# Kernel optimization log

Measured on AMD Instinct MI355X. Metric: run time of the kernel, lower is better.

The kernel has to match this reference:

```python
import jax, jax.numpy as jnp
import numpy as np

D_MODEL, D_STATE, D_CONV, EXPAND = 1024, 16, 4, 2
D_INNER = EXPAND * D_MODEL            # 2048
DT_RANK = -(-D_MODEL // 16)           # ceil(d_model/16) = 64


def setup_inputs() -> dict:
    key = jax.random.key(0)
    ks = jax.random.split(key, 9)
    B, L = 2, 2048
    x = jax.random.normal(ks[0], (B, L, D_MODEL), dtype=jnp.float32)
    s = 0.02
    W_in = jax.random.normal(ks[1], (2 * D_INNER, D_MODEL), dtype=jnp.float32) * s
    conv_w = jax.random.normal(ks[2], (D_INNER, 1, D_CONV), dtype=jnp.float32) * 0.1
    conv_b = jax.random.normal(ks[3], (D_INNER,), dtype=jnp.float32) * 0.01
    W_xproj = jax.random.normal(ks[4], (DT_RANK + 2 * D_STATE, D_INNER), dtype=jnp.float32) * s
    W_dt = jax.random.normal(ks[5], (D_INNER, DT_RANK), dtype=jnp.float32) * (DT_RANK ** -0.5)
    b_dt = jnp.log(jnp.exp(jax.random.uniform(ks[6], (D_INNER,), minval=1e-3, maxval=0.1)) - 1.0)  # inv-softplus init
    A_log = jnp.log(jnp.broadcast_to(jnp.arange(1, D_STATE + 1, dtype=jnp.float32), (D_INNER, D_STATE)))
    Dskip = jnp.ones((D_INNER,), dtype=jnp.float32)
    W_out = jax.random.normal(ks[7], (D_MODEL, D_INNER), dtype=jnp.float32) * s
    return {"x": x, "W_in": W_in, "conv_w": conv_w, "conv_b": conv_b,
            "W_xproj": W_xproj, "W_dt": W_dt, "b_dt": b_dt,
            "A_log": A_log, "Dskip": Dskip, "W_out": W_out}


def _mamba_fwd(x, W_in, conv_w, conv_b, W_xproj, W_dt, b_dt, A_log, Dskip, W_out):
    Bsz, L, _ = x.shape
    # in_proj -> split into x branch and gate z
    xz = jnp.einsum('bld,ed->ble', x, W_in)               # (B,L,2*d_inner)
    xb, z = jnp.split(xz, 2, axis=-1)
    # causal depthwise conv1d over time
    xc = jnp.transpose(xb, (0, 2, 1))                      # (B,d_inner,L)
    xc = jax.lax.conv_general_dilated(
        xc, conv_w, window_strides=(1,), padding=[(D_CONV - 1, 0)],
        dimension_numbers=('NCH', 'OIH', 'NCH'), feature_group_count=D_INNER)
    u = jax.nn.silu(jnp.transpose(xc, (0, 2, 1)) + conv_b)  # (B,L,d_inner)
    # input-dependent SSM params
    x_dbl = jnp.einsum('bld,ed->ble', u, W_xproj)          # (B,L,dt_rank+2n)
    dt_low, Bmat, Cmat = jnp.split(x_dbl, [DT_RANK, DT_RANK + D_STATE], axis=-1)
    delta = jax.nn.softplus(jnp.einsum('blr,dr->bld', dt_low, W_dt) + b_dt)  # (B,L,d_inner)
    A = -jnp.exp(A_log)                                    # (d_inner,d_state)

    def step(h, inp):
        dt_t, u_t, B_t, C_t = inp                          # (B,d),(B,d),(B,n),(B,n)
        dA = jnp.exp(dt_t[:, :, None] * A)                 # (B,d,n)
        h = dA * h + (dt_t * u_t)[:, :, None] * B_t[:, None, :]
        y_t = jnp.einsum('bdn,bn->bd', h, C_t)
        return h, y_t

    h0 = jnp.zeros((Bsz, D_INNER, D_STATE), dtype=x.dtype)
    xs = (jnp.transpose(delta, (1, 0, 2)), jnp.transpose(u, (1, 0, 2)),
          jnp.transpose(Bmat, (1, 0, 2)), jnp.transpose(Cmat, (1, 0, 2)))
    _, ys = jax.lax.scan(step, h0, xs)                     # (L,B,d_inner)
    y = jnp.transpose(ys, (1, 0, 2)) + u * Dskip           # skip connection
    y = y * jax.nn.silu(z)                                 # gating
    return jnp.einsum('bld,ed->ble', y, W_out)             # (B,L,d_model)


def reference(x, W_in, conv_w, conv_b, W_xproj, W_dt, b_dt, A_log, Dskip, W_out):
    return _mamba_fwd(x, W_in, conv_w, conv_b, W_xproj, W_dt, b_dt, A_log, Dskip, W_out)
```

## Files before the change

kernel.cpp:

```cpp
#include <hip/hip_runtime.h>
#include <math.h>

#define MB_B      2
#define MB_L      2048
#define MB_DMODEL 1024
#define MB_DINNER 2048
#define MB_DSTATE 16
#define MB_DTRANK 64
#define MB_ROWS   (MB_B * MB_L)
#define MB_E2     (2 * MB_DINNER)
#define SC_NC     32
#define SC_CHUNK  (MB_L / SC_NC)
#define SC_CL     32
#define SC_CB     64
#define CV_R      4

typedef _Float16 f16;
typedef __attribute__((ext_vector_type(2))) _Float16 half2v;
typedef __attribute__((ext_vector_type(4))) _Float16 half4;
typedef __attribute__((ext_vector_type(8))) _Float16 half8;
typedef __attribute__((ext_vector_type(4))) float floatx4;

__device__ __forceinline__ float softplus_f(float x) {
    return (x > 20.f) ? x : log1pf(expf(x));
}
__device__ __forceinline__ float silu_f(float x) {
    return x / (1.f + expf(-x));
}

#if __has_builtin(__builtin_amdgcn_exp2f)
__device__ __forceinline__ float exp2_fast(float x) {
    return __builtin_amdgcn_exp2f(x);
}
#else
__device__ __forceinline__ float exp2_fast(float x) {
    return __expf(0.69314718056f * x);
}
#endif

typedef const __attribute__((address_space(1))) unsigned char gbyte;
typedef __attribute__((address_space(3))) unsigned char lbyte;
__device__ __forceinline__ void gl_lds16(const void* g, void* l) {
    __builtin_amdgcn_global_load_lds((gbyte*)g, (lbyte*)l, 16, 0, 0);
}

template <int CTRL>
__device__ __forceinline__ float dpp_add(float x) {
    int xi = __builtin_bit_cast(int, x);
    int yi = __builtin_amdgcn_update_dpp(0, xi, CTRL, 0xF, 0xF, true);
    return x + __builtin_bit_cast(float, yi);
}

__global__ __launch_bounds__(256) void convert_all_kernel(
    const float* __restrict__ x, const float* __restrict__ W_in,
    const float* __restrict__ W_xproj, const float* __restrict__ W_dt,
    const float* __restrict__ W_out, f16* __restrict__ dst)
{
    const int i = (blockIdx.x * 256 + threadIdx.x) * 8;
    const float* src;
    int local, nsrc;
    if (i < 4194304)      { src = x;       local = i;           nsrc = 4194304; }
    else if (i < 8388608) { src = W_in;    local = i - 4194304; nsrc = 4194304; }
    else if (i < 8650752) { src = W_xproj; local = i - 8388608; nsrc = 196608; }
    else if (i < 8781824) { src = W_dt;    local = i - 8650752; nsrc = 131072; }
    else                  { src = W_out;   local = i - 8781824; nsrc = 2097152; }
    half8 o;
    if (local < nsrc) {
        const float4 a = *reinterpret_cast<const float4*>(src + local);
        const float4 b = *reinterpret_cast<const float4*>(src + local + 4);
        o[0] = (f16)a.x; o[1] = (f16)a.y; o[2] = (f16)a.z; o[3] = (f16)a.w;
        o[4] = (f16)b.x; o[5] = (f16)b.y; o[6] = (f16)b.z; o[7] = (f16)b.w;
    } else {
#pragma unroll
        for (int j = 0; j < 8; j++) o[j] = (f16)0.f;
    }
    *reinterpret_cast<half8*>(dst + i) = o;
}

template <typename OutT, int EPI, int BM, int GN>
__global__ __launch_bounds__(256) void gemm_mfma(
    const f16* __restrict__ A, int lda,
    const f16* __restrict__ B, int ldb,
    OutT* __restrict__ C, int ldc, int K,
    const float* __restrict__ bias)
{
    constexpr int BN = 128;
    constexpr int GM = 4 / GN;
    constexpr int WM = BM / GM;
    constexpr int WN = BN / GN;
    constexpr int MT = WM / 16, NT = WN / 16;
    constexpr int CPW = (BM + BN) / 32;

    __shared__ f16 As[BM * 64];
    __shared__ f16 Bs[BN * 64];

    const int tid  = threadIdx.x;
    const int lane = tid & 63;
    const int wave = tid >> 6;
    const int wr   = wave / GN, wc = wave % GN;
    const int bm   = blockIdx.y * BM, bn = blockIdx.x * BN;

    floatx4 zero4 = {0.f, 0.f, 0.f, 0.f};
    floatx4 acc[MT][NT];
#pragma unroll
    for (int i = 0; i < MT; i++)
#pragma unroll
        for (int j = 0; j < NT; j++) acc[i][j] = zero4;

    const int srow = lane >> 3;
    const int scol = ((lane & 7) ^ (srow & 7)) * 8;
    const f16* gp[CPW];
    f16* lp[CPW];
#pragma unroll
    for (int i = 0; i < CPW; i++) {
        const int rbase = (wave * CPW + i) * 8;
        if (rbase < BM) {
            gp[i] = A + (size_t)(bm + rbase + srow) * lda + scol;
            lp[i] = As + rbase * 64;
        } else {
            gp[i] = B + (size_t)(bn + (rbase - BM) + srow) * ldb + scol;
            lp[i] = Bs + (rbase - BM) * 64;
        }
    }

    const int mr = lane & 15;
    const int ko = lane >> 4;

    for (int k0 = 0; k0 < K; k0 += 64) {
#pragma unroll
        for (int i = 0; i < CPW; i++) gl_lds16(gp[i] + k0, lp[i]);
        __syncthreads();

        half8 af[MT][2], bf[NT][2];
#pragma unroll
        for (int kk = 0; kk < 2; kk++) {
            const int koff = ((ko + kk * 4) ^ (mr & 7)) * 8;
#pragma unroll
            for (int mt = 0; mt < MT; mt++)
                af[mt][kk] = *reinterpret_cast<const half8*>(
                    As + (wr * WM + mt * 16 + mr) * 64 + koff);
#pragma unroll
            for (int nt = 0; nt < NT; nt++)
                bf[nt][kk] = *reinterpret_cast<const half8*>(
                    Bs + (wc * WN + nt * 16 + mr) * 64 + koff);
        }
#pragma unroll
        for (int kk = 0; kk < 2; kk++)
#pragma unroll
            for (int mt = 0; mt < MT; mt++)
#pragma unroll
                for (int nt = 0; nt < NT; nt++)
                    acc[mt][nt] = __builtin_amdgcn_mfma_f32_16x16x32_f16(
                        af[mt][kk], bf[nt][kk], acc[mt][nt], 0, 0, 0);
        __syncthreads();
    }

    const int rbase = (lane >> 4) * 4;
#pragma unroll
    for (int mt = 0; mt < MT; mt++) {
        const int row0 = bm + wr * WM + mt * 16 + rbase;
#pragma unroll
        for (int nt = 0; nt < NT; nt++) {
            const int col = bn + wc * WN + nt * 16 + mr;
#pragma unroll
            for (int r = 0; r < 4; r++) {
                float v = acc[mt][nt][r];
                if constexpr (EPI == 1) v = softplus_f(v + bias[col]);
                C[(size_t)(row0 + r) * ldc + col] = (OutT)v;
            }
        }
    }
}

__global__ __launch_bounds__(256) void gemm3_splitk(
    const f16* __restrict__ A, const f16* __restrict__ B,
    float* __restrict__ Cp)
{
    __shared__ f16 As[128 * 32];
    __shared__ f16 Bs[128 * 32];

    const int tid  = threadIdx.x;
    const int lane = tid & 63;
    const int wave = tid >> 6;
    const int wr   = wave >> 1, wc = wave & 1;
    const int bm   = blockIdx.y * 128;
    const int kbeg = blockIdx.x * 256;

    floatx4 zero4 = {0.f, 0.f, 0.f, 0.f};
    floatx4 acc[4][4];
#pragma unroll
    for (int i = 0; i < 4; i++)
#pragma unroll
        for (int j = 0; j < 4; j++) acc[i][j] = zero4;

    const int srow = lane >> 2;
    const int scol = ((lane & 3) ^ ((srow >> 1) & 3)) * 8;
    const f16* gA0 = A + (size_t)(bm + wave * 32 + srow) * MB_DINNER + scol;
    const f16* gA1 = A + (size_t)(bm + wave * 32 + 16 + srow) * MB_DINNER + scol;
    const f16* gB0 = B + (size_t)(wave * 32 + srow) * MB_DINNER + scol;
    const f16* gB1 = B + (size_t)(wave * 32 + 16 + srow) * MB_DINNER + scol;
    f16* lA0 = As + wave * 1024;
    f16* lA1 = As + wave * 1024 + 512;
    f16* lB0 = Bs + wave * 1024;
    f16* lB1 = Bs + wave * 1024 + 512;

    const int mr = lane & 15;
    const int kq = ((lane >> 4) ^ ((mr >> 1) & 3)) * 8;

    for (int k0 = kbeg; k0 < kbeg + 256; k0 += 32) {
        gl_lds16(gA0 + k0, lA0);
        gl_lds16(gA1 + k0, lA1);
        gl_lds16(gB0 + k0, lB0);
        gl_lds16(gB1 + k0, lB1);
        __syncthreads();

        half8 af[4], bf[4];
#pragma unroll
        for (int mt = 0; mt < 4; mt++)
            af[mt] = *reinterpret_cast<const half8*>(
                As + (wr * 64 + mt * 16 + mr) * 32 + kq);
#pragma unroll
        for (int nt = 0; nt < 4; nt++)
            bf[nt] = *reinterpret_cast<const half8*>(
                Bs + (wc * 64 + nt * 16 + mr) * 32 + kq);
#pragma unroll
        for (int mt = 0; mt < 4; mt++)
#pragma unroll
            for (int nt = 0; nt < 4; nt++)
                acc[mt][nt] = __builtin_amdgcn_mfma_f32_16x16x32_f16(
                    af[mt], bf[nt], acc[mt][nt], 0, 0, 0);
        __syncthreads();
    }

    float* Co = Cp + (size_t)blockIdx.x * MB_ROWS * 128;
    const int rbase = (lane >> 4) * 4;
#pragma unroll
    for (int mt = 0; mt < 4; mt++) {
        const int row0 = bm + wr * 64 + mt * 16 + rbase;
#pragma unroll
        for (int nt = 0; nt < 4; nt++) {
            const int col = wc * 64 + nt * 16 + mr;
#pragma unroll
            for (int r = 0; r < 4; r++)
                Co[(size_t)(row0 + r) * 128 + col] = acc[mt][nt][r];
        }
    }
}

__global__ __launch_bounds__(256) void reduce_xdbl_kernel(
    const float* __restrict__ Cp, float* __restrict__ xdbl,
    f16* __restrict__ xdbl_h)
{
    const int t = blockIdx.x * 256 + threadIdx.x;
    const int row = t >> 5, c4 = (t & 31) * 4;
    float4 s = {0.f, 0.f, 0.f, 0.f};
#pragma unroll
    for (int j = 0; j < 8; j++) {
        const float4 v = *reinterpret_cast<const float4*>(
            Cp + (size_t)j * MB_ROWS * 128 + (size_t)row * 128 + c4);
        s.x += v.x; s.y += v.y; s.z += v.z; s.w += v.w;
    }
    if (c4 < 96)
        *reinterpret_cast<float4*>(xdbl + (size_t)row * 96 + c4) = s;
    half4 h = {(f16)s.x, (f16)s.y, (f16)s.z, (f16)s.w};
    *reinterpret_cast<half4*>(xdbl_h + (size_t)row * 128 + c4) = h;
}

__global__ __launch_bounds__(256) void conv_silu_kernel(
    const f16* __restrict__ xz, const float* __restrict__ cw,
    const float* __restrict__ cb, f16* __restrict__ u)
{
    const int tid  = threadIdx.x;
    const int dv   = tid * 8;
    const int rbeg = blockIdx.x * CV_R;
    const int l0   = rbeg & (MB_L - 1);

    float wt[8][4];
#pragma unroll
    for (int j = 0; j < 8; j++) {
        const float4 wv = *reinterpret_cast<const float4*>(cw + (dv + j) * 4);
        wt[j][0] = wv.x; wt[j][1] = wv.y; wt[j][2] = wv.z; wt[j][3] = wv.w;
    }
    float bias[8];
    {
        const float4 b0 = *reinterpret_cast<const float4*>(cb + dv);
        const float4 b1 = *reinterpret_cast<const float4*>(cb + dv + 4);
        bias[0] = b0.x; bias[1] = b0.y; bias[2] = b0.z; bias[3] = b0.w;
        bias[4] = b1.x; bias[5] = b1.y; bias[6] = b1.z; bias[7] = b1.w;
    }

    half8 xr[CV_R + 3];
#pragma unroll
    for (int i = 0; i < 3; i++) {
        if (l0 >= 3 - i) {
            xr[i] = *reinterpret_cast<const half8*>(
                xz + (size_t)(rbeg - 3 + i) * MB_E2 + dv);
        } else {
#pragma unroll
            for (int j = 0; j < 8; j++) xr[i][j] = (f16)0.f;
        }
    }
#pragma unroll
    for (int r = 0; r < CV_R; r++)
        xr[3 + r] = *reinterpret_cast<const half8*>(
            xz + (size_t)(rbeg + r) * MB_E2 + dv);

#pragma unroll
    for (int r = 0; r < CV_R; r++) {
        float acc[8];
#pragma unroll
        for (int j = 0; j < 8; j++) acc[j] = bias[j];
#pragma unroll
        for (int k = 0; k < 4; k++) {
            const half8 xv = xr[r + k];
#pragma unroll
            for (int j = 0; j < 8; j++)
                acc[j] = fmaf((float)xv[j], wt[j][k], acc[j]);
        }
        half8 o;
#pragma unroll
        for (int j = 0; j < 8; j++) o[j] = (f16)silu_f(acc[j]);
        *reinterpret_cast<half8*>(u + (size_t)(rbeg + r) * MB_DINNER + dv) = o;
    }
}

__global__ __launch_bounds__(256) void scan_pass1(
    const f16*  __restrict__ delta,
    const f16*  __restrict__ u,
    const float* __restrict__ xdbl,
    const float* __restrict__ A_log,
    float* __restrict__ Hc,
    float* __restrict__ Pc)
{
    __shared__ half2v sDU[SC_CB][SC_CL + 2];
    __shared__ float  sB[SC_CL][20];

    const int tid   = threadIdx.x;
    const int lane  = tid & 63;
    const int wave  = tid >> 6;
    const int cg    = (lane >> 2) & 15;
    const int q     = lane & 3;
    const int ch    = wave * 16 + cg;
    const int cb    = blockIdx.x & 63;
    const int chunk = blockIdx.x >> 6;
    const int gchan = cb * SC_CB + ch;
    const int b     = gchan >> 11;
    const int dbase = (cb & 31) * SC_CB;
    const int d     = dbase + ch;
    const int lbeg  = chunk * SC_CHUNK;

    const size_t base2048 = (size_t)b * MB_L * MB_DINNER;
    const size_t base96   = (size_t)b * MB_L * 96;

    const float4 alog = *reinterpret_cast<const float4*>(
        A_log + d * MB_DSTATE + q * 4);
    float Av2[4] = {-expf(alog.x) * 1.44269504f, -expf(alog.y) * 1.44269504f,
                    -expf(alog.z) * 1.44269504f, -expf(alog.w) * 1.44269504f};
    float h[4] = {0.f, 0.f, 0.f, 0.f};
    float sdt = 0.f;

    const int lloc  = tid >> 3;
    const int c8    = (tid & 7) * 8;
    const int cpair = (tid & 7) * 2;

    half8 pD, pU; float2 pB;
    auto stage_load = [&](int l0) {
        const size_t row = (size_t)(l0 + lloc);
        pD = *reinterpret_cast<const half8*>(
            delta + base2048 + row * MB_DINNER + dbase + c8);
        pU = *reinterpret_cast<const half8*>(
            u + base2048 + row * MB_DINNER + dbase + c8);
        pB = *reinterpret_cast<const float2*>(
            xdbl + base96 + row * 96 + MB_DTRANK + cpair);
    };
    auto stage_write = [&]() {
#pragma unroll
        for (int j = 0; j < 8; j++) {
            half2v t; t[0] = pD[j]; t[1] = pD[j] * pU[j];
            sDU[c8 + j][lloc] = t;
        }
        *reinterpret_cast<float2*>(&sB[lloc][cpair]) = pB;
    };

    stage_load(lbeg);
    stage_write();
    __syncthreads();

    for (int l0 = lbeg; l0 < lbeg + SC_CHUNK; l0 += SC_CL) {
        const bool has_next = (l0 + SC_CL) < lbeg + SC_CHUNK;
        if (has_next) stage_load(l0 + SC_CL);

#pragma unroll
        for (int ll = 0; ll < SC_CL; ll++) {
            const half2v duh = sDU[ch][ll];
            const float dx = (float)duh[0], dy = (float)duh[1];
            const float4 Bv = *reinterpret_cast<const float4*>(&sB[ll][q * 4]);
            h[0] = fmaf(exp2_fast(dx * Av2[0]), h[0], dy * Bv.x);
            h[1] = fmaf(exp2_fast(dx * Av2[1]), h[1], dy * Bv.y);
            h[2] = fmaf(exp2_fast(dx * Av2[2]), h[2], dy * Bv.z);
            h[3] = fmaf(exp2_fast(dx * Av2[3]), h[3], dy * Bv.w);
            sdt += dx;
        }
        __syncthreads();
        if (has_next) stage_write();
        __syncthreads();
    }

    const size_t cidx = ((size_t)chunk * MB_ROWS + gchan) * MB_DSTATE + q * 4;
    float4 H4 = {h[0], h[1], h[2], h[3]};
    float4 P4 = {exp2_fast(Av2[0] * sdt), exp2_fast(Av2[1] * sdt),
                 exp2_fast(Av2[2] * sdt), exp2_fast(Av2[3] * sdt)};
    *reinterpret_cast<float4*>(Hc + cidx) = H4;
    *reinterpret_cast<float4*>(Pc + cidx) = P4;
}

__global__ __launch_bounds__(256) void scan_pass2(
    const f16*  __restrict__ delta,
    const f16*  __restrict__ u,
    const float* __restrict__ xdbl,
    const float* __restrict__ A_log,
    const float* __restrict__ Dskip,
    const f16*  __restrict__ xz,
    const float* __restrict__ Hc,
    const float* __restrict__ Pc,
    f16* __restrict__ yg)
{
    __shared__ half2v sDU[SC_CB][SC_CL + 2];
    __shared__ half2v sGS[SC_CB][SC_CL + 2];
    __shared__ float  sB[SC_CL][20];
    __shared__ float  sC[SC_CL][20];

    const int tid   = threadIdx.x;
    const int lane  = tid & 63;
    const int wave  = tid >> 6;
    const int cg    = (lane >> 2) & 15;
    const int q     = lane & 3;
    const int ch    = wave * 16 + cg;
    const int cb    = blockIdx.x & 63;
    const int chunk = blockIdx.x >> 6;
    const int gchan = cb * SC_CB + ch;
    const int b     = gchan >> 11;
    const int dbase = (cb & 31) * SC_CB;
    const int d     = dbase + ch;
    const int lbeg  = chunk * SC_CHUNK;

    const size_t base2048 = (size_t)b * MB_L * MB_DINNER;
    const size_t base4096 = (size_t)b * MB_L * MB_E2;
    const size_t base96   = (size_t)b * MB_L * 96;

    const float4 alog = *reinterpret_cast<const float4*>(
        A_log + d * MB_DSTATE + q * 4);
    float Av2[4] = {-expf(alog.x) * 1.44269504f, -expf(alog.y) * 1.44269504f,
                    -expf(alog.z) * 1.44269504f, -expf(alog.w) * 1.44269504f};

    const int lloc  = tid >> 3;
    const int c8    = (tid & 7) * 8;
    const int cpair = (tid & 7) * 2;

    float Dsk8[8];
    {
        const float4 d0 = *reinterpret_cast<const float4*>(Dskip + dbase + c8);
        const float4 d1 = *reinterpret_cast<const float4*>(Dskip + dbase + c8 + 4);
        Dsk8[0] = d0.x; Dsk8[1] = d0.y; Dsk8[2] = d0.z; Dsk8[3] = d0.w;
        Dsk8[4] = d1.x; Dsk8[5] = d1.y; Dsk8[6] = d1.z; Dsk8[7] = d1.w;
    }

    half8 pD, pU, pZ; float2 pB, pC;
    auto stage_load = [&](int l0) {
        const size_t row = (size_t)(l0 + lloc);
        pD = *reinterpret_cast<const half8*>(
            delta + base2048 + row * MB_DINNER + dbase + c8);
        pU = *reinterpret_cast<const half8*>(
            u + base2048 + row * MB_DINNER + dbase + c8);
        pZ = *reinterpret_cast<const half8*>(
            xz + base4096 + row * MB_E2 + MB_DINNER + dbase + c8);
        pB = *reinterpret_cast<const float2*>(
            xdbl + base96 + row * 96 + MB_DTRANK + cpair);
        pC = *reinterpret_cast<const float2*>(
            xdbl + base96 + row * 96 + MB_DTRANK + MB_DSTATE + cpair);
    };
    auto stage_write = [&]() {
#pragma unroll
        for (int j = 0; j < 8; j++) {
            half2v t; t[0] = pD[j]; t[1] = pD[j] * pU[j];
            sDU[c8 + j][lloc] = t;
            const float uu = (float)pU[j];
            const float g = silu_f((float)pZ[j]);
            half2v gs; gs[0] = (f16)g; gs[1] = (f16)(uu * Dsk8[j] * g);
            sGS[c8 + j][lloc] = gs;
        }
        *reinterpret_cast<float2*>(&sB[lloc][cpair]) = pB;
        *reinterpret_cast<float2*>(&sC[lloc][cpair]) = pC;
    };

    stage_load(lbeg);

    float h[4] = {0.f, 0.f, 0.f, 0.f};
    for (int j = 0; j < chunk; j++) {
        const size_t cidx = ((size_t)j * MB_ROWS + gchan) * MB_DSTATE + q * 4;
        const float4 P4 = *reinterpret_cast<const float4*>(Pc + cidx);
        const float4 H4 = *reinterpret_cast<const float4*>(Hc + cidx);
        h[0] = fmaf(P4.x, h[0], H4.x);
        h[1] = fmaf(P4.y, h[1], H4.y);
        h[2] = fmaf(P4.z, h[2], H4.z);
        h[3] = fmaf(P4.w, h[3], H4.w);
    }

    stage_write();
    __syncthreads();

    for (int l0 = lbeg; l0 < lbeg + SC_CHUNK; l0 += SC_CL) {
        const bool has_next = (l0 + SC_CL) < lbeg + SC_CHUNK;
        if (has_next) stage_load(l0 + SC_CL);

        float y[SC_CL / 4] = {0.f, 0.f, 0.f, 0.f, 0.f, 0.f, 0.f, 0.f};
#pragma unroll
        for (int ll = 0; ll < SC_CL; ll++) {
            const half2v duh = sDU[ch][ll];
            const float dx = (float)duh[0], dy = (float)duh[1];
            const float4 Bv = *reinterpret_cast<const float4*>(&sB[ll][q * 4]);
            const float4 Cv = *reinterpret_cast<const float4*>(&sC[ll][q * 4]);
            h[0] = fmaf(exp2_fast(dx * Av2[0]), h[0], dy * Bv.x);
            h[1] = fmaf(exp2_fast(dx * Av2[1]), h[1], dy * Bv.y);
            h[2] = fmaf(exp2_fast(dx * Av2[2]), h[2], dy * Bv.z);
            h[3] = fmaf(exp2_fast(dx * Av2[3]), h[3], dy * Bv.w);
            float p = h[0] * Cv.x;
            p = fmaf(h[1], Cv.y, p);
            p = fmaf(h[2], Cv.z, p);
            p = fmaf(h[3], Cv.w, p);
            p = dpp_add<0xB1>(p);
            p = dpp_add<0x4E>(p);
            y[ll >> 2] = (q == (ll & 3)) ? p : y[ll >> 2];
        }

#pragma unroll
        for (int k = 0; k < SC_CL / 4; k++) {
            const half2v gs = sGS[ch][4 * k + q];
            yg[base2048 + (size_t)(l0 + 4 * k + q) * MB_DINNER + dbase + ch] =
                (f16)fmaf(y[k], (float)gs[0], (float)gs[1]);
        }

        __syncthreads();
        if (has_next) stage_write();
        __syncthreads();
    }
}

extern "C" void kernel_launch(void* const* d_in, const int* in_sizes, int n_in,
                              void* d_out, int out_size, void* d_ws,
                              size_t ws_size, hipStream_t stream)
{
    const float* x      = (const float*)d_in[0];
    const float* W_in   = (const float*)d_in[1];
    const float* conv_w = (const float*)d_in[2];
    const float* conv_b = (const float*)d_in[3];
    const float* W_xproj= (const float*)d_in[4];
    const float* W_dt   = (const float*)d_in[5];
    const float* b_dt   = (const float*)d_in[6];
    const float* A_log  = (const float*)d_in[7];
    const float* Dskip  = (const float*)d_in[8];
    const float* W_out  = (const float*)d_in[9];
    float* out = (float*)d_out;

    char* p = (char*)d_ws;
    f16* xz_h    = (f16*)p;  p += (size_t)MB_ROWS * MB_E2 * 2;
    f16* u_h     = (f16*)p;  p += (size_t)MB_ROWS * MB_DINNER * 2;
    f16* delta_h = (f16*)p;  p += (size_t)MB_ROWS * MB_DINNER * 2;
    f16* yg_h    = (f16*)p;  p += (size_t)MB_ROWS * MB_DINNER * 2;
    float* xdbl  = (float*)p; p += (size_t)MB_ROWS * 96 * 4;
    f16* xdbl_h  = (f16*)p;  p += (size_t)MB_ROWS * 128 * 2;
    f16* x_h     = (f16*)p;  p += (size_t)MB_ROWS * MB_DMODEL * 2;
    f16* W_inh   = (f16*)p;  p += (size_t)MB_E2 * MB_DMODEL * 2;
    f16* W_xprojh= (f16*)p;  p += (size_t)128 * MB_DINNER * 2;
    f16* W_dth   = (f16*)p;  p += (size_t)MB_DINNER * MB_DTRANK * 2;
    f16* W_outh  = (f16*)p;  p += (size_t)MB_DMODEL * MB_DINNER * 2;
    float* Cp    = (float*)p;
    float* Hc    = Cp;
    float* Pc    = Cp + (size_t)SC_NC * MB_ROWS * MB_DSTATE;

    const dim3 blk(256);

    convert_all_kernel<<<5312, blk, 0, stream>>>(
        x, W_in, W_xproj, W_dt, W_out, x_h);

    gemm_mfma<f16, 0, 128, 2><<<dim3(32, 32), blk, 0, stream>>>(
        x_h, MB_DMODEL, W_inh, MB_DMODEL, xz_h, MB_E2, MB_DMODEL, nullptr);

    conv_silu_kernel<<<MB_ROWS / CV_R, blk, 0, stream>>>(
        xz_h, conv_w, conv_b, u_h);

    gemm3_splitk<<<dim3(8, 32), blk, 0, stream>>>(u_h, W_xprojh, Cp);
    reduce_xdbl_kernel<<<512, blk, 0, stream>>>(Cp, xdbl, xdbl_h);

    gemm_mfma<f16, 1, 128, 2><<<dim3(16, 32), blk, 0, stream>>>(
        xdbl_h, 128, W_dth, MB_DTRANK, delta_h, MB_DINNER, MB_DTRANK, b_dt);

    scan_pass1<<<(SC_NC - 1) * 64, blk, 0, stream>>>(
        delta_h, u_h, xdbl, A_log, Hc, Pc);

    scan_pass2<<<SC_NC * 64, blk, 0, stream>>>(
        delta_h, u_h, xdbl, A_log, Dskip, xz_h, Hc, Pc, yg_h);

    gemm_mfma<float, 0, 64, 4><<<dim3(8, 64), blk, 0, stream>>>(
        yg_h, MB_DINNER, W_outh, MB_DINNER, out, MB_DMODEL, MB_DINNER, nullptr);
}
```

Baseline: 308.7 us.

## Store split-K partials in fp16, split dt/BC outputs, remap in_proj block order

```diff
diff --git a/kernel.cpp b/kernel.cpp
--- a/kernel.cpp
+++ b/kernel.cpp
@@ -77,11 +77,11 @@
     *reinterpret_cast<half8*>(dst + i) = o;
 }
 
-template <typename OutT, int EPI, int BM, int GN>
+template <typename OutT, int EPI, int BM, int GN, int CMLOG>
 __global__ __launch_bounds__(256) void gemm_mfma(
     const f16* __restrict__ A, int lda,
     const f16* __restrict__ B, int ldb,
-    OutT* __restrict__ C, int ldc, int K,
+    OutT* __restrict__ C, int ldc, int kiters, long stepA, long stepB,
     const float* __restrict__ bias)
 {
     constexpr int BN = 128;
@@ -98,7 +98,16 @@
     const int lane = tid & 63;
     const int wave = tid >> 6;
     const int wr   = wave / GN, wc = wave % GN;
-    const int bm   = blockIdx.y * BM, bn = blockIdx.x * BN;
+
+    int bxi, byi;
+    if constexpr (CMLOG >= 0) {
+        const int n = blockIdx.x;
+        byi = ((n & 7) << CMLOG) | ((n >> 3) & ((1 << CMLOG) - 1));
+        bxi = n >> (3 + CMLOG);
+    } else {
+        bxi = blockIdx.x; byi = blockIdx.y;
+    }
+    const int bm = byi * BM, bn = bxi * BN;
 
     floatx4 zero4 = {0.f, 0.f, 0.f, 0.f};
     floatx4 acc[MT][NT];
@@ -111,24 +120,28 @@
     const int scol = ((lane & 7) ^ (srow & 7)) * 8;
     const f16* gp[CPW];
     f16* lp[CPW];
+    long stp[CPW];
 #pragma unroll
     for (int i = 0; i < CPW; i++) {
         const int rbase = (wave * CPW + i) * 8;
         if (rbase < BM) {
             gp[i] = A + (size_t)(bm + rbase + srow) * lda + scol;
             lp[i] = As + rbase * 64;
+            stp[i] = stepA;
         } else {
             gp[i] = B + (size_t)(bn + (rbase - BM) + srow) * ldb + scol;
             lp[i] = Bs + (rbase - BM) * 64;
+            stp[i] = stepB;
         }
     }
 
     const int mr = lane & 15;
     const int ko = lane >> 4;
 
-    for (int k0 = 0; k0 < K; k0 += 64) {
-#pragma unroll
-        for (int i = 0; i < CPW; i++) gl_lds16(gp[i] + k0, lp[i]);
+    for (int it = 0; it < kiters; it++) {
+#pragma unroll
+        for (int i = 0; i < CPW; i++)
+            gl_lds16(gp[i] + (size_t)((long)it * stp[i]), lp[i]);
         __syncthreads();
 
         half8 af[MT][2], bf[NT][2];
@@ -174,7 +187,7 @@
 
 __global__ __launch_bounds__(256) void gemm3_splitk(
     const f16* __restrict__ A, const f16* __restrict__ B,
-    float* __restrict__ Cp)
+    f16* __restrict__ Cp)
 {
     __shared__ f16 As[128 * 32];
     __shared__ f16 Bs[128 * 32];
@@ -232,7 +245,7 @@
         __syncthreads();
     }
 
-    float* Co = Cp + (size_t)blockIdx.x * MB_ROWS * 128;
+    f16* Co = Cp + (size_t)blockIdx.x * MB_ROWS * 128;
     const int rbase = (lane >> 4) * 4;
 #pragma unroll
     for (int mt = 0; mt < 4; mt++) {
@@ -242,28 +255,41 @@
             const int col = wc * 64 + nt * 16 + mr;
 #pragma unroll
             for (int r = 0; r < 4; r++)
-                Co[(size_t)(row0 + r) * 128 + col] = acc[mt][nt][r];
-        }
-    }
-}
-
-__global__ __launch_bounds__(256) void reduce_xdbl_kernel(
-    const float* __restrict__ Cp, float* __restrict__ xdbl,
-    f16* __restrict__ xdbl_h)
+                Co[(size_t)(row0 + r) * 128 + col] = (f16)acc[mt][nt][r];
+        }
+    }
+}
+
+__global__ __launch_bounds__(256) void reduce_bc_kernel(
+    const f16* __restrict__ Cp, f16* __restrict__ dt_h,
+    float* __restrict__ bc)
 {
     const int t = blockIdx.x * 256 + threadIdx.x;
-    const int row = t >> 5, c4 = (t & 31) * 4;
-    float4 s = {0.f, 0.f, 0.f, 0.f};
-#pragma unroll
-    for (int j = 0; j < 8; j++) {
-        const float4 v = *reinterpret_cast<const float4*>(
-            Cp + (size_t)j * MB_ROWS * 128 + (size_t)row * 128 + c4);
-        s.x += v.x; s.y += v.y; s.z += v.z; s.w += v.w;
-    }
-    if (c4 < 96)
-        *reinterpret_cast<float4*>(xdbl + (size_t)row * 96 + c4) = s;
-    half4 h = {(f16)s.x, (f16)s.y, (f16)s.z, (f16)s.w};
-    *reinterpret_cast<half4*>(xdbl_h + (size_t)row * 128 + c4) = h;
+    if (t < 65536) {
+        const int row = t >> 4, c4 = (t & 15) * 4;
+        float s[4] = {0.f, 0.f, 0.f, 0.f};
+#pragma unroll
+        for (int j = 0; j < 8; j++) {
+            const half4 v = *reinterpret_cast<const half4*>(
+                Cp + (size_t)j * MB_ROWS * 128 + (size_t)row * 128 + c4);
+            s[0] += (float)v[0]; s[1] += (float)v[1];
+            s[2] += (float)v[2]; s[3] += (float)v[3];
+        }
+        half4 h = {(f16)s[0], (f16)s[1], (f16)s[2], (f16)s[3]};
+        *reinterpret_cast<half4*>(dt_h + (size_t)row * 64 + c4) = h;
+    } else {
+        const int t2 = t - 65536;
+        const int row = t2 >> 3, c4 = (t2 & 7) * 4;
+        float4 s = {0.f, 0.f, 0.f, 0.f};
+#pragma unroll
+        for (int j = 0; j < 8; j++) {
+            const half4 v = *reinterpret_cast<const half4*>(
+                Cp + (size_t)j * MB_ROWS * 128 + (size_t)row * 128 + 64 + c4);
+            s.x += (float)v[0]; s.y += (float)v[1];
+            s.z += (float)v[2]; s.w += (float)v[3];
+        }
+        *reinterpret_cast<float4*>(bc + (size_t)row * 32 + c4) = s;
+    }
 }
 
 __global__ __launch_bounds__(256) void conv_silu_kernel(
@@ -327,7 +353,7 @@
 __global__ __launch_bounds__(256) void scan_pass1(
     const f16*  __restrict__ delta,
     const f16*  __restrict__ u,
-    const float* __restrict__ xdbl,
+    const float* __restrict__ bc,
     const float* __restrict__ A_log,
     float* __restrict__ Hc,
     float* __restrict__ Pc)
@@ -350,7 +376,7 @@
     const int lbeg  = chunk * SC_CHUNK;
 
     const size_t base2048 = (size_t)b * MB_L * MB_DINNER;
-    const size_t base96   = (size_t)b * MB_L * 96;
+    const size_t baseBC   = (size_t)b * MB_L * 32;
 
     const float4 alog = *reinterpret_cast<const float4*>(
         A_log + d * MB_DSTATE + q * 4);
@@ -370,8 +396,7 @@
             delta + base2048 + row * MB_DINNER + dbase + c8);
         pU = *reinterpret_cast<const half8*>(
             u + base2048 + row * MB_DINNER + dbase + c8);
-        pB = *reinterpret_cast<const float2*>(
-            xdbl + base96 + row * 96 + MB_DTRANK + cpair);
+        pB = *reinterpret_cast<const float2*>(bc + baseBC + row * 32 + cpair);
     };
     auto stage_write = [&]() {
 #pragma unroll
@@ -417,7 +442,7 @@
 __global__ __launch_bounds__(256) void scan_pass2(
     const f16*  __restrict__ delta,
     const f16*  __restrict__ u,
-    const float* __restrict__ xdbl,
+    const float* __restrict__ bc,
     const float* __restrict__ A_log,
     const float* __restrict__ Dskip,
     const f16*  __restrict__ xz,
@@ -446,7 +471,7 @@
 
     const size_t base2048 = (size_t)b * MB_L * MB_DINNER;
     const size_t base4096 = (size_t)b * MB_L * MB_E2;
-    const size_t base96   = (size_t)b * MB_L * 96;
+    const size_t baseBC   = (size_t)b * MB_L * 32;
 
     const float4 alog = *reinterpret_cast<const float4*>(
         A_log + d * MB_DSTATE + q * 4);
@@ -474,10 +499,9 @@
             u + base2048 + row * MB_DINNER + dbase + c8);
         pZ = *reinterpret_cast<const half8*>(
             xz + base4096 + row * MB_E2 + MB_DINNER + dbase + c8);
-        pB = *reinterpret_cast<const float2*>(
-            xdbl + base96 + row * 96 + MB_DTRANK + cpair);
+        pB = *reinterpret_cast<const float2*>(bc + baseBC + row * 32 + cpair);
         pC = *reinterpret_cast<const float2*>(
-            xdbl + base96 + row * 96 + MB_DTRANK + MB_DSTATE + cpair);
+            bc + baseBC + row * 32 + 16 + cpair);
     };
     auto stage_write = [&]() {
 #pragma unroll
@@ -567,40 +591,41 @@
     f16* u_h     = (f16*)p;  p += (size_t)MB_ROWS * MB_DINNER * 2;
     f16* delta_h = (f16*)p;  p += (size_t)MB_ROWS * MB_DINNER * 2;
     f16* yg_h    = (f16*)p;  p += (size_t)MB_ROWS * MB_DINNER * 2;
-    float* xdbl  = (float*)p; p += (size_t)MB_ROWS * 96 * 4;
-    f16* xdbl_h  = (f16*)p;  p += (size_t)MB_ROWS * 128 * 2;
     f16* x_h     = (f16*)p;  p += (size_t)MB_ROWS * MB_DMODEL * 2;
     f16* W_inh   = (f16*)p;  p += (size_t)MB_E2 * MB_DMODEL * 2;
     f16* W_xprojh= (f16*)p;  p += (size_t)128 * MB_DINNER * 2;
     f16* W_dth   = (f16*)p;  p += (size_t)MB_DINNER * MB_DTRANK * 2;
     f16* W_outh  = (f16*)p;  p += (size_t)MB_DMODEL * MB_DINNER * 2;
-    float* Cp    = (float*)p;
-    float* Hc    = Cp;
-    float* Pc    = Cp + (size_t)SC_NC * MB_ROWS * MB_DSTATE;
+    f16* Cp_h    = (f16*)p;  p += (size_t)8 * MB_ROWS * 128 * 2;
+    f16* dt_h    = (f16*)p;  p += (size_t)MB_ROWS * 64 * 2;
+    float* bc    = (float*)p; p += (size_t)MB_ROWS * 32 * 4;
+    float* Hc    = (float*)p; p += (size_t)SC_NC * MB_ROWS * MB_DSTATE * 4;
+    float* Pc    = (float*)p;
 
     const dim3 blk(256);
 
     convert_all_kernel<<<5312, blk, 0, stream>>>(
         x, W_in, W_xproj, W_dt, W_out, x_h);
 
-    gemm_mfma<f16, 0, 128, 2><<<dim3(32, 32), blk, 0, stream>>>(
-        x_h, MB_DMODEL, W_inh, MB_DMODEL, xz_h, MB_E2, MB_DMODEL, nullptr);
+    gemm_mfma<f16, 0, 128, 2, 2><<<1024, blk, 0, stream>>>(
+        x_h, MB_DMODEL, W_inh, MB_DMODEL, xz_h, MB_E2, 16, 64, 64, nullptr);
 
     conv_silu_kernel<<<MB_ROWS / CV_R, blk, 0, stream>>>(
         xz_h, conv_w, conv_b, u_h);
 
-    gemm3_splitk<<<dim3(8, 32), blk, 0, stream>>>(u_h, W_xprojh, Cp);
-    reduce_xdbl_kernel<<<512, blk, 0, stream>>>(Cp, xdbl, xdbl_h);
-
-    gemm_mfma<f16, 1, 128, 2><<<dim3(16, 32), blk, 0, stream>>>(
-        xdbl_h, 128, W_dth, MB_DTRANK, delta_h, MB_DINNER, MB_DTRANK, b_dt);
+    gemm3_splitk<<<dim3(8, 32), blk, 0, stream>>>(u_h, W_xprojh, Cp_h);
+    reduce_bc_kernel<<<384, blk, 0, stream>>>(Cp_h, dt_h, bc);
+
+    gemm_mfma<f16, 1, 128, 2, -1><<<dim3(16, 32), blk, 0, stream>>>(
+        dt_h, 64, W_dth, MB_DTRANK, delta_h, MB_DINNER, 1, 64, 64, b_dt);
 
     scan_pass1<<<(SC_NC - 1) * 64, blk, 0, stream>>>(
-        delta_h, u_h, xdbl, A_log, Hc, Pc);
+        delta_h, u_h, bc, A_log, Hc, Pc);
 
     scan_pass2<<<SC_NC * 64, blk, 0, stream>>>(
-        delta_h, u_h, xdbl, A_log, Dskip, xz_h, Hc, Pc, yg_h);
-
-    gemm_mfma<float, 0, 64, 4><<<dim3(8, 64), blk, 0, stream>>>(
-        yg_h, MB_DINNER, W_outh, MB_DINNER, out, MB_DMODEL, MB_DINNER, nullptr);
-}
+        delta_h, u_h, bc, A_log, Dskip, xz_h, Hc, Pc, yg_h);
+
+    gemm_mfma<float, 0, 64, 4, -1><<<dim3(8, 64), blk, 0, stream>>>(
+        yg_h, MB_DINNER, W_outh, MB_DINNER, out, MB_DMODEL, 32, 64, 64,
+        nullptr);
+}
```

Result: slower. 316.5 us (+2.5%).
